# Kernel tuning notes

Hardware: AMD Instinct MI355X
Metric: run time of the kernel (lower is better)

## Reference

```python
import jax, jax.numpy as jnp
import numpy as np

DIM = 1024
INNER = int(DIM * 1.5)
EPS = 1e-6


def setup_inputs() -> dict:
    key = jax.random.key(0)
    ks = jax.random.split(key, 8)
    B, L, D = 4, 2048, DIM
    s1 = 1.0 / np.sqrt(D)
    s2 = 1.0 / np.sqrt(INNER)
    return {
        "x": jax.random.normal(ks[0], (B, L, D), jnp.float32),
        "W1": jax.random.normal(ks[1], (D, INNER), jnp.float32) * s1,
        "b1": jnp.zeros((INNER,), jnp.float32),
        "W2": jax.random.normal(ks[2], (INNER, 3 * D), jnp.float32) * s2,
        "b2": jnp.zeros((3 * D,), jnp.float32),
        "Wv": jax.random.normal(ks[3], (D, D), jnp.float32) * (0.5 * s1),
        "bv": jnp.zeros((D,), jnp.float32),
        "mix_weight": jnp.full((D,), 0.5, jnp.float32),
        "norm_weight": jnp.ones((D,), jnp.float32),
    }


def rmsnorm(x, w):
    norm = jnp.sqrt(jnp.mean(x * x, axis=-1, keepdims=True) + EPS)
    return x / norm * w


def reference(x, W1, b1, W2, b2, Wv, bv, mix_weight, norm_weight):
    B, L, D = x.shape
    h = jax.nn.silu(x @ W1 + b1)              # [B,L,inner]
    qkg = h @ W2 + b2                          # [B,L,3D]
    q, k, g = jnp.split(qkg, 3, axis=-1)
    scores = jnp.einsum('bld,bmd->blm', q, k) / jnp.sqrt(jnp.float32(D))
    attn = jax.nn.softmax(scores, axis=-1)
    v = (x @ Wv + bv) * jax.nn.sigmoid(g)      # gated values [B,L,D]
    global_info = jnp.einsum('blm,bmd->bld', attn, v)
    output = mix_weight * global_info + (1.0 - mix_weight) * x
    return rmsnorm(output, norm_weight)
```

## Files before the change

### kernel.cpp

```cpp
#include <hip/hip_runtime.h>
#include <hip/hip_bf16.h>
#include <stdint.h>


typedef __bf16 bf16x8 __attribute__((ext_vector_type(8)));
typedef float f32x4 __attribute__((ext_vector_type(4)));

__device__ __forceinline__ unsigned short f2bf(float f) {
    unsigned int u = __float_as_uint(f);
    u += 0x7fffu + ((u >> 16) & 1u);
    return (unsigned short)(u >> 16);
}
__device__ __forceinline__ float bf2f(unsigned short s) {
    return __uint_as_float(((unsigned int)s) << 16);
}
__device__ __forceinline__ void llds16(const void* g, void* l) {
    __builtin_amdgcn_global_load_lds(
        (const __attribute__((address_space(1))) void*)g,
        (__attribute__((address_space(3))) void*)l, 16, 0, 0);
}

__global__ __launch_bounds__(256) void cvt_f32_bf16(
    const float* __restrict__ in, unsigned short* __restrict__ out, long long n8) {
    long long i = (long long)blockIdx.x * 256 + threadIdx.x;
    if (i >= n8) return;
    float4 a = ((const float4*)in)[2 * i];
    float4 b = ((const float4*)in)[2 * i + 1];
    ushort4 p0, p1;
    p0.x = f2bf(a.x); p0.y = f2bf(a.y); p0.z = f2bf(a.z); p0.w = f2bf(a.w);
    p1.x = f2bf(b.x); p1.y = f2bf(b.y); p1.z = f2bf(b.z); p1.w = f2bf(b.w);
    ((ushort4*)out)[2 * i] = p0;
    ((ushort4*)out)[2 * i + 1] = p1;
}

__global__ __launch_bounds__(256) void transpose_cvt(
    const float* __restrict__ in, unsigned short* __restrict__ out, int R, int C) {
    __shared__ unsigned short tile[32][33];
    int c0 = blockIdx.x * 32, r0 = blockIdx.y * 32;
    int cc = threadIdx.x & 31, rr = threadIdx.x >> 5;
#pragma unroll
    for (int p = 0; p < 4; ++p) {
        int r = rr + p * 8;
        tile[r][cc] = f2bf(in[(size_t)(r0 + r) * C + c0 + cc]);
    }
    __syncthreads();
#pragma unroll
    for (int p = 0; p < 4; ++p) {
        int c = rr + p * 8;
        out[(size_t)(c0 + c) * R + r0 + cc] = tile[cc][c];
    }
}

template <int EPI>
__global__ __launch_bounds__(512, 1) void gemm3(
    const unsigned short* __restrict__ A, int lda, long long Abs,
    const unsigned short* __restrict__ B, int ldb, long long Bbs,
    int K,
    void* __restrict__ out, int ldo, long long Obs,
    const float* __restrict__ bias,
    const unsigned short* __restrict__ gate, int ldg,
    const float* __restrict__ xres, const float* __restrict__ mix,
    float scale) {
    extern __shared__ unsigned short lds[];
    constexpr int BUFU = 24576;
    const int tid = threadIdx.x;
    const int lane = tid & 63, wid = tid >> 6;
    const int wr = wid >> 1, wc = wid & 1;
    const int bm = blockIdx.y * 256, bn = blockIdx.x * 128;
    const int z = blockIdx.z;
    A += (long long)z * Abs;
    B += (long long)z * Bbs;
    const int NT = K >> 6;

    const int sr = tid >> 3, ss = tid & 7;
    size_t ag[4], bg[2];
#pragma unroll
    for (int j = 0; j < 4; ++j) {
        int r = j * 64 + sr;
        ag[j] = (size_t)(bm + r) * lda + (size_t)((ss ^ (r & 7)) * 8);
    }
#pragma unroll
    for (int j = 0; j < 2; ++j) {
        int r = j * 64 + sr;
        bg[j] = (size_t)(bn + r) * ldb + (size_t)((ss ^ (r & 7)) * 8);
    }
    const int aL = wid * 512;

    const int arow = wr * 64 + (lane & 15);
    const int brow = wc * 64 + (lane & 15);
    const int g4 = lane >> 4;
    const int sx0 = ((g4 ^ (lane & 7)) * 8);
    const int sx1 = (((4 + g4) ^ (lane & 7)) * 8);

    f32x4 acc[4][4] = {};

#pragma unroll
    for (int j = 0; j < 4; ++j) llds16(A + ag[j], &lds[j * 4096 + aL]);
#pragma unroll
    for (int j = 0; j < 2; ++j) llds16(B + bg[j], &lds[16384 + j * 4096 + aL]);
#pragma unroll
    for (int j = 0; j < 4; ++j) llds16(A + ag[j] + 64, &lds[BUFU + j * 4096 + aL]);
#pragma unroll
    for (int j = 0; j < 2; ++j)
        llds16(B + bg[j] + 64, &lds[BUFU + 16384 + j * 4096 + aL]);
    asm volatile("s_waitcnt vmcnt(6)" ::: "memory");
    __builtin_amdgcn_s_barrier();

    int bb = 0;
    for (int t = 0; t < NT; ++t) {
        const bool st = (t + 2 < NT);
        if (st) {
            const int tgt = (bb >= BUFU) ? bb - BUFU : bb + 2 * BUFU;
            const size_t k0 = (size_t)(t + 2) << 6;
#pragma unroll
            for (int j = 0; j < 4; ++j)
                llds16(A + ag[j] + k0, &lds[tgt + j * 4096 + aL]);
#pragma unroll
            for (int j = 0; j < 2; ++j)
                llds16(B + bg[j] + k0, &lds[tgt + 16384 + j * 4096 + aL]);
        }
        __builtin_amdgcn_sched_barrier(0);
        const unsigned short* Ab = &lds[bb];
        const unsigned short* Bb = &lds[bb + 16384];
        bf16x8 a0[4], a1[4], b0[4], b1[4];
#pragma unroll
        for (int i = 0; i < 4; ++i) {
            a0[i] = *(const bf16x8*)&Ab[(arow + i * 16) * 64 + sx0];
            a1[i] = *(const bf16x8*)&Ab[(arow + i * 16) * 64 + sx1];
            b0[i] = *(const bf16x8*)&Bb[(brow + i * 16) * 64 + sx0];
            b1[i] = *(const bf16x8*)&Bb[(brow + i * 16) * 64 + sx1];
        }
#pragma unroll
        for (int i = 0; i < 4; ++i)
#pragma unroll
            for (int j = 0; j < 4; ++j)
                acc[i][j] = __builtin_amdgcn_mfma_f32_16x16x32_bf16(
                    a0[i], b0[j], acc[i][j], 0, 0, 0);
#pragma unroll
        for (int i = 0; i < 4; ++i)
#pragma unroll
            for (int j = 0; j < 4; ++j)
                acc[i][j] = __builtin_amdgcn_mfma_f32_16x16x32_bf16(
                    a1[i], b1[j], acc[i][j], 0, 0, 0);
        asm volatile("s_waitcnt lgkmcnt(0)" ::: "memory");
        if (st) asm volatile("s_waitcnt vmcnt(6)" ::: "memory");
        else    asm volatile("s_waitcnt vmcnt(0)" ::: "memory");
        __builtin_amdgcn_s_barrier();
        bb = (bb == 2 * BUFU) ? 0 : bb + BUFU;
    }

    const int row0 = bm + wr * 64, col0 = bn + wc * 64;
#pragma unroll
    for (int i = 0; i < 4; ++i) {
#pragma unroll
        for (int j = 0; j < 4; ++j) {
            const int n = col0 + j * 16 + (lane & 15);
            const int mb = row0 + i * 16 + ((lane >> 4) << 2);
            f32x4 v = acc[i][j];
            if constexpr (EPI == 0 || EPI == 1) {
                float bs = bias[n];
                unsigned short* o = (unsigned short*)out;
#pragma unroll
                for (int q = 0; q < 4; ++q) {
                    float val = v[q] + bs;
                    if constexpr (EPI == 0) val = val / (1.f + __expf(-val));
                    o[(size_t)(mb + q) * ldo + n] = f2bf(val);
                }
            } else if constexpr (EPI == 2) {
                float bs = bias[n];
                ushort4 pk;
                unsigned short* pku = (unsigned short*)&pk;
#pragma unroll
                for (int q = 0; q < 4; ++q) {
                    int m = mb + q;
                    float g = bf2f(gate[(size_t)m * ldg + n]);
                    float val = (v[q] + bs) / (1.f + __expf(-g));
                    pku[q] = f2bf(val);
                }
                unsigned short* o = (unsigned short*)out;
                size_t oi = ((size_t)(mb >> 11) * 1024 + n) * 2048 + (mb & 2047);
                *(ushort4*)(o + oi) = pk;
            } else if constexpr (EPI == 3) {
                float* o = (float*)out + (size_t)z * Obs;
#pragma unroll
                for (int q = 0; q < 4; ++q)
                    o[(size_t)(mb + q) * ldo + n] = v[q] * scale;
            } else {
                float* o = (float*)out + (size_t)z * Obs;
                const float* xr = xres + (size_t)z * Obs;
                float mw = mix[n];
#pragma unroll
                for (int q = 0; q < 4; ++q)
                    o[(size_t)(mb + q) * ldo + n] =
                        mw * v[q] + (1.f - mw) * xr[(size_t)(mb + q) * ldo + n];
            }
        }
    }
}

__global__ __launch_bounds__(256) void softmax_inplace(float* __restrict__ scores) {
    const int L = 2048;
    float* sr = scores + (size_t)blockIdx.x * L;
    const int t = threadIdx.x, lane = t & 63, wid = t >> 6;
    float4 a = ((const float4*)sr)[2 * t];
    float4 b = ((const float4*)sr)[2 * t + 1];
    float vv[8] = {a.x, a.y, a.z, a.w, b.x, b.y, b.z, b.w};
    float mx = vv[0];
#pragma unroll
    for (int i = 1; i < 8; ++i) mx = fmaxf(mx, vv[i]);
#pragma unroll
    for (int off = 32; off; off >>= 1) mx = fmaxf(mx, __shfl_xor(mx, off));
    __shared__ float redm[4], reds[4];
    if (lane == 0) redm[wid] = mx;
    __syncthreads();
    mx = fmaxf(fmaxf(redm[0], redm[1]), fmaxf(redm[2], redm[3]));
    float s = 0.f;
#pragma unroll
    for (int i = 0; i < 8; ++i) {
        vv[i] = __expf(vv[i] - mx);
        s += vv[i];
    }
#pragma unroll
    for (int off = 32; off; off >>= 1) s += __shfl_xor(s, off);
    if (lane == 0) reds[wid] = s;
    __syncthreads();
    s = reds[0] + reds[1] + reds[2] + reds[3];
    float inv = 1.f / s;
    ushort4 p0, p1;
    unsigned short* pp0 = (unsigned short*)&p0;
    unsigned short* pp1 = (unsigned short*)&p1;
#pragma unroll
    for (int i = 0; i < 4; ++i) pp0[i] = f2bf(vv[i] * inv);
#pragma unroll
    for (int i = 0; i < 4; ++i) pp1[i] = f2bf(vv[4 + i] * inv);
    unsigned short* pr = (unsigned short*)sr;
    ((ushort4*)pr)[2 * t] = p0;
    ((ushort4*)pr)[2 * t + 1] = p1;
}

__global__ __launch_bounds__(256) void rmsnorm_inplace(
    float* __restrict__ io, const float* __restrict__ w) {
    const int D = 1024;
    float* r = io + (size_t)blockIdx.x * D;
    const int t = threadIdx.x, lane = t & 63, wid = t >> 6;
    float4 v = ((const float4*)r)[t];
    float ss = v.x * v.x + v.y * v.y + v.z * v.z + v.w * v.w;
#pragma unroll
    for (int off = 32; off; off >>= 1) ss += __shfl_xor(ss, off);
    __shared__ float red[4];
    if (lane == 0) red[wid] = ss;
    __syncthreads();
    ss = red[0] + red[1] + red[2] + red[3];
    float sc = rsqrtf(ss / (float)D + 1e-6f);
    float4 wv = ((const float4*)w)[t];
    v.x *= sc * wv.x; v.y *= sc * wv.y; v.z *= sc * wv.z; v.w *= sc * wv.w;
    ((float4*)r)[t] = v;
}

extern "C" void kernel_launch(void* const* d_in, const int* in_sizes, int n_in,
                              void* d_out, int out_size, void* d_ws, size_t ws_size,
                              hipStream_t stream) {
    const float* x = (const float*)d_in[0];
    const float* W1 = (const float*)d_in[1];
    const float* b1 = (const float*)d_in[2];
    const float* W2 = (const float*)d_in[3];
    const float* b2 = (const float*)d_in[4];
    const float* Wv = (const float*)d_in[5];
    const float* bv = (const float*)d_in[6];
    const float* mixw = (const float*)d_in[7];
    const float* normw = (const float*)d_in[8];
    float* out = (float*)d_out;

    const int L = 2048, D = 1024, INNER = 1536, BN4 = 4;
    const int M = BN4 * L;
    const int SMEM = 147456;

    (void)hipFuncSetAttribute(reinterpret_cast<const void*>(&gemm3<0>),
                              hipFuncAttributeMaxDynamicSharedMemorySize, SMEM);
    (void)hipFuncSetAttribute(reinterpret_cast<const void*>(&gemm3<1>),
                              hipFuncAttributeMaxDynamicSharedMemorySize, SMEM);
    (void)hipFuncSetAttribute(reinterpret_cast<const void*>(&gemm3<2>),
                              hipFuncAttributeMaxDynamicSharedMemorySize, SMEM);
    (void)hipFuncSetAttribute(reinterpret_cast<const void*>(&gemm3<3>),
                              hipFuncAttributeMaxDynamicSharedMemorySize, SMEM);
    (void)hipFuncSetAttribute(reinterpret_cast<const void*>(&gemm3<4>),
                              hipFuncAttributeMaxDynamicSharedMemorySize, SMEM);

    char* w = (char*)d_ws;
    auto carve = [&](size_t bytes) {
        void* p = (void*)w;
        w += (bytes + 255) & ~(size_t)255;
        return p;
    };
    unsigned short* xbf = (unsigned short*)carve((size_t)M * D * 2);
    unsigned short* w1t = (unsigned short*)carve((size_t)INNER * D * 2);
    unsigned short* w2t = (unsigned short*)carve((size_t)3 * D * INNER * 2);
    unsigned short* wvt = (unsigned short*)carve((size_t)D * D * 2);
    unsigned short* h = (unsigned short*)carve((size_t)M * INNER * 2);
    unsigned short* qkg = (unsigned short*)carve((size_t)M * 3 * D * 2);
    unsigned short* vt = (unsigned short*)carve((size_t)BN4 * D * L * 2);
    float* scores = (float*)carve((size_t)BN4 * L * L * 4);

    cvt_f32_bf16<<<(M * D) / 2048, 256, 0, stream>>>(x, xbf, (long long)M * D / 8);
    transpose_cvt<<<dim3(INNER / 32, D / 32), 256, 0, stream>>>(W1, w1t, D, INNER);
    transpose_cvt<<<dim3(3 * D / 32, INNER / 32), 256, 0, stream>>>(W2, w2t, INNER, 3 * D);
    transpose_cvt<<<dim3(D / 32, D / 32), 256, 0, stream>>>(Wv, wvt, D, D);
    gemm3<0><<<dim3(INNER / 128, M / 256, 1), 512, SMEM, stream>>>(
        xbf, D, 0, w1t, D, 0, D, h, INNER, 0, b1, nullptr, 0, nullptr, nullptr, 1.f);
    gemm3<1><<<dim3(3 * D / 128, M / 256, 1), 512, SMEM, stream>>>(
        h, INNER, 0, w2t, INNER, 0, INNER, qkg, 3 * D, 0, b2, nullptr, 0, nullptr,
        nullptr, 1.f);
    gemm3<2><<<dim3(D / 128, M / 256, 1), 512, SMEM, stream>>>(
        xbf, D, 0, wvt, D, 0, D, vt, L, 0, bv, qkg + 2 * D, 3 * D, nullptr, nullptr,
        1.f);
    gemm3<3><<<dim3(L / 128, L / 256, BN4), 512, SMEM, stream>>>(
        qkg, 3 * D, (long long)L * 3 * D, qkg + D, 3 * D, (long long)L * 3 * D, D,
        scores, L, (long long)L * L, nullptr, nullptr, 0, nullptr, nullptr, 0.03125f);
    softmax_inplace<<<BN4 * L, 256, 0, stream>>>(scores);
    gemm3<4><<<dim3(D / 128, L / 256, BN4), 512, SMEM, stream>>>(
        (const unsigned short*)scores, 2 * L, (long long)L * 2 * L, vt, L,
        (long long)D * L, L, out, D, (long long)L * D, nullptr, nullptr, 0, x, mixw,
        1.f);
    rmsnorm_inplace<<<M, 256, 0, stream>>>(out, normw);
}
```

Baseline: 311.0 us.

## Add 256x256-tile GEMM kernel with interleaved LDS prefetch for three GEMMs

Adds a new gemm8 kernel that uses 256x256 output tiles (8 waves, each 128x64) instead of 128x256. It double-buffers A and B in LDS and spreads the global-to-LDS loads across four sub-phases of each k-step, with setprio around the MFMA blocks. The W1, W2 and QK^T GEMMs now use this kernel, which raises arithmetic intensity per loaded byte and halves the grid size. The cost is more accumulator registers (128 floats per thread) and fewer blocks for the smaller GEMMs, which could hurt occupancy or tail behaviour.

```diff
diff --git a/kernel.cpp b/kernel.cpp
--- a/kernel.cpp
+++ b/kernel.cpp
@@ -48,6 +48,145 @@
     for (int p = 0; p < 4; ++p) {
         int c = rr + p * 8;
         out[(size_t)(c0 + c) * R + r0 + cc] = tile[cc][c];
+    }
+}
+
+template <int EPI>
+__global__ __launch_bounds__(512, 1) void gemm8(
+    const unsigned short* __restrict__ A, int lda, long long Abs,
+    const unsigned short* __restrict__ B, int ldb, long long Bbs,
+    int K,
+    void* __restrict__ out, int ldo, long long Obs,
+    const float* __restrict__ bias, float scale) {
+    extern __shared__ unsigned short lds[];
+    const int tid = threadIdx.x, lane = tid & 63, wid = tid >> 6;
+    const int wr = wid >> 2, wc = wid & 3;
+    const int bm = blockIdx.y * 256, bn = blockIdx.x * 256;
+    const int z = blockIdx.z;
+    A += (long long)z * Abs;
+    B += (long long)z * Bbs;
+    const int NT = K >> 6;
+
+    const int srow = tid >> 3;
+    const int swz = ((tid & 7) ^ (srow & 7)) * 8;
+    size_t ga[2][2], gb[2][2];
+#pragma unroll
+    for (int h = 0; h < 2; ++h)
+#pragma unroll
+        for (int c = 0; c < 2; ++c) {
+            ga[h][c] = (size_t)(bm + h * 128 + c * 64 + srow) * lda + swz;
+            gb[h][c] = (size_t)(bn + h * 128 + c * 64 + srow) * ldb + swz;
+        }
+    const int wl = wid * 512;
+
+    auto stA = [&](int k0, int h, int bb) {
+        llds16(A + ga[h][0] + k0, &lds[bb + h * 8192 + wl]);
+        llds16(A + ga[h][1] + k0, &lds[bb + h * 8192 + 4096 + wl]);
+    };
+    auto stB = [&](int k0, int h, int bb) {
+        llds16(B + gb[h][0] + k0, &lds[bb + 16384 + h * 8192 + wl]);
+        llds16(B + gb[h][1] + k0, &lds[bb + 16384 + h * 8192 + 4096 + wl]);
+    };
+
+    const int l15 = lane & 15, g4 = lane >> 4, l7 = lane & 7;
+    const int xs0 = (g4 ^ l7) * 8;
+    const int xs1 = ((4 + g4) ^ l7) * 8;
+    const int abase = wr * 8192 + l15 * 64;
+    const int bbase = 16384 + (wc >> 1) * 8192 + (wc & 1) * 4096 + l15 * 64;
+
+    f32x4 acc[8][4] = {};
+
+    stA(0, 0, 0); stA(0, 1, 0); stB(0, 0, 0); stB(0, 1, 0);
+    stB(64, 0, 32768); stB(64, 1, 32768);
+    asm volatile("s_waitcnt vmcnt(4)" ::: "memory");
+    __builtin_amdgcn_s_barrier();
+
+    for (int kt = 0; kt < NT; kt += 2) {
+        const bool st2 = (kt + 2) < NT;
+        const int kA1 = (kt + 1) << 6;
+        const int kN2 = (kt + 2) << 6;
+        const int kN3 = (kt + 3) << 6;
+#pragma unroll
+        for (int hb = 0; hb < 2; ++hb) {
+            const int bb = hb * 32768;
+            bf16x8 bfr[4][2];
+            bf16x8 afr[2][2];
+#pragma unroll
+            for (int q = 0; q < 4; ++q) {
+                if (q == 0) {
+#pragma unroll
+                    for (int n = 0; n < 4; ++n) {
+                        bfr[n][0] = *(const bf16x8*)&lds[bb + bbase + n * 1024 + xs0];
+                        bfr[n][1] = *(const bf16x8*)&lds[bb + bbase + n * 1024 + xs1];
+                    }
+                }
+#pragma unroll
+                for (int mq = 0; mq < 2; ++mq) {
+                    afr[mq][0] =
+                        *(const bf16x8*)&lds[bb + abase + (q * 2 + mq) * 1024 + xs0];
+                    afr[mq][1] =
+                        *(const bf16x8*)&lds[bb + abase + (q * 2 + mq) * 1024 + xs1];
+                }
+                if (hb == 0) {
+                    if (q == 0) stA(kA1, 0, 32768);
+                    else if (q == 1) stA(kA1, 1, 32768);
+                    else if (q == 2) { if (st2) stB(kN2, 0, 0); }
+                    else { if (st2) stB(kN2, 1, 0); }
+                } else {
+                    if (q == 0) { if (st2) stA(kN2, 0, 0); }
+                    else if (q == 1) { if (st2) stA(kN2, 1, 0); }
+                    else if (q == 2) { if (st2) stB(kN3, 0, 32768); }
+                    else { if (st2) stB(kN3, 1, 32768); }
+                }
+                __builtin_amdgcn_s_barrier();
+                asm volatile("s_waitcnt lgkmcnt(0)" ::: "memory");
+                __builtin_amdgcn_sched_barrier(0);
+                __builtin_amdgcn_s_setprio(1);
+#pragma unroll
+                for (int s = 0; s < 2; ++s)
+#pragma unroll
+                    for (int mq = 0; mq < 2; ++mq)
+#pragma unroll
+                        for (int n = 0; n < 4; ++n)
+                            acc[q * 2 + mq][n] =
+                                __builtin_amdgcn_mfma_f32_16x16x32_bf16(
+                                    afr[mq][s], bfr[n][s], acc[q * 2 + mq][n],
+                                    0, 0, 0);
+                __builtin_amdgcn_s_setprio(0);
+                __builtin_amdgcn_sched_barrier(0);
+                if (q == 3) {
+                    if (st2) asm volatile("s_waitcnt vmcnt(4)" ::: "memory");
+                    else     asm volatile("s_waitcnt vmcnt(0)" ::: "memory");
+                }
+                __builtin_amdgcn_s_barrier();
+            }
+        }
+    }
+
+    const int row0 = bm + wr * 128, col0 = bn + wc * 64;
+#pragma unroll
+    for (int m = 0; m < 8; ++m) {
+#pragma unroll
+        for (int n = 0; n < 4; ++n) {
+            const int nn = col0 + n * 16 + l15;
+            const int mb = row0 + m * 16 + g4 * 4;
+            f32x4 v = acc[m][n];
+            if constexpr (EPI == 0 || EPI == 1) {
+                float bs = bias[nn];
+                unsigned short* o = (unsigned short*)out;
+#pragma unroll
+                for (int qq = 0; qq < 4; ++qq) {
+                    float val = v[qq] + bs;
+                    if constexpr (EPI == 0) val = val / (1.f + __expf(-val));
+                    o[(size_t)(mb + qq) * ldo + nn] = f2bf(val);
+                }
+            } else {
+                float* o = (float*)out + (size_t)z * Obs;
+#pragma unroll
+                for (int qq = 0; qq < 4; ++qq)
+                    o[(size_t)(mb + qq) * ldo + nn] = v[qq] * scale;
+            }
+        }
     }
 }
 
@@ -157,16 +296,7 @@
             const int n = col0 + j * 16 + (lane & 15);
             const int mb = row0 + i * 16 + ((lane >> 4) << 2);
             f32x4 v = acc[i][j];
-            if constexpr (EPI == 0 || EPI == 1) {
-                float bs = bias[n];
-                unsigned short* o = (unsigned short*)out;
-#pragma unroll
-                for (int q = 0; q < 4; ++q) {
-                    float val = v[q] + bs;
-                    if constexpr (EPI == 0) val = val / (1.f + __expf(-val));
-                    o[(size_t)(mb + q) * ldo + n] = f2bf(val);
-                }
-            } else if constexpr (EPI == 2) {
+            if constexpr (EPI == 2) {
                 float bs = bias[n];
                 ushort4 pk;
                 unsigned short* pku = (unsigned short*)&pk;
@@ -180,11 +310,6 @@
                 unsigned short* o = (unsigned short*)out;
                 size_t oi = ((size_t)(mb >> 11) * 1024 + n) * 2048 + (mb & 2047);
                 *(ushort4*)(o + oi) = pk;
-            } else if constexpr (EPI == 3) {
-                float* o = (float*)out + (size_t)z * Obs;
-#pragma unroll
-                for (int q = 0; q < 4; ++q)
-                    o[(size_t)(mb + q) * ldo + n] = v[q] * scale;
             } else {
                 float* o = (float*)out + (size_t)z * Obs;
                 const float* xr = xres + (size_t)z * Obs;
@@ -273,18 +398,19 @@
 
     const int L = 2048, D = 1024, INNER = 1536, BN4 = 4;
     const int M = BN4 * L;
-    const int SMEM = 147456;
-
-    (void)hipFuncSetAttribute(reinterpret_cast<const void*>(&gemm3<0>),
-                              hipFuncAttributeMaxDynamicSharedMemorySize, SMEM);
-    (void)hipFuncSetAttribute(reinterpret_cast<const void*>(&gemm3<1>),
-                              hipFuncAttributeMaxDynamicSharedMemorySize, SMEM);
+    const int SMEM3 = 147456;
+    const int SMEM8 = 131072;
+
+    (void)hipFuncSetAttribute(reinterpret_cast<const void*>(&gemm8<0>),
+                              hipFuncAttributeMaxDynamicSharedMemorySize, SMEM8);
+    (void)hipFuncSetAttribute(reinterpret_cast<const void*>(&gemm8<1>),
+                              hipFuncAttributeMaxDynamicSharedMemorySize, SMEM8);
+    (void)hipFuncSetAttribute(reinterpret_cast<const void*>(&gemm8<3>),
+                              hipFuncAttributeMaxDynamicSharedMemorySize, SMEM8);
     (void)hipFuncSetAttribute(reinterpret_cast<const void*>(&gemm3<2>),
-                              hipFuncAttributeMaxDynamicSharedMemorySize, SMEM);
-    (void)hipFuncSetAttribute(reinterpret_cast<const void*>(&gemm3<3>),
-                              hipFuncAttributeMaxDynamicSharedMemorySize, SMEM);
+                              hipFuncAttributeMaxDynamicSharedMemorySize, SMEM3);
     (void)hipFuncSetAttribute(reinterpret_cast<const void*>(&gemm3<4>),
-                              hipFuncAttributeMaxDynamicSharedMemorySize, SMEM);
+                              hipFuncAttributeMaxDynamicSharedMemorySize, SMEM3);
 
     char* w = (char*)d_ws;
     auto carve = [&](size_t bytes) {
@@ -305,19 +431,18 @@
     transpose_cvt<<<dim3(INNER / 32, D / 32), 256, 0, stream>>>(W1, w1t, D, INNER);
     transpose_cvt<<<dim3(3 * D / 32, INNER / 32), 256, 0, stream>>>(W2, w2t, INNER, 3 * D);
     transpose_cvt<<<dim3(D / 32, D / 32), 256, 0, stream>>>(Wv, wvt, D, D);
-    gemm3<0><<<dim3(INNER / 128, M / 256, 1), 512, SMEM, stream>>>(
-        xbf, D, 0, w1t, D, 0, D, h, INNER, 0, b1, nullptr, 0, nullptr, nullptr, 1.f);
-    gemm3<1><<<dim3(3 * D / 128, M / 256, 1), 512, SMEM, stream>>>(
-        h, INNER, 0, w2t, INNER, 0, INNER, qkg, 3 * D, 0, b2, nullptr, 0, nullptr,
-        nullptr, 1.f);
-    gemm3<2><<<dim3(D / 128, M / 256, 1), 512, SMEM, stream>>>(
+    gemm8<0><<<dim3(INNER / 256, M / 256, 1), 512, SMEM8, stream>>>(
+        xbf, D, 0, w1t, D, 0, D, h, INNER, 0, b1, 1.f);
+    gemm8<1><<<dim3(3 * D / 256, M / 256, 1), 512, SMEM8, stream>>>(
+        h, INNER, 0, w2t, INNER, 0, INNER, qkg, 3 * D, 0, b2, 1.f);
+    gemm3<2><<<dim3(D / 128, M / 256, 1), 512, SMEM3, stream>>>(
         xbf, D, 0, wvt, D, 0, D, vt, L, 0, bv, qkg + 2 * D, 3 * D, nullptr, nullptr,
         1.f);
-    gemm3<3><<<dim3(L / 128, L / 256, BN4), 512, SMEM, stream>>>(
+    gemm8<3><<<dim3(L / 256, L / 256, BN4), 512, SMEM8, stream>>>(
         qkg, 3 * D, (long long)L * 3 * D, qkg + D, 3 * D, (long long)L * 3 * D, D,
-        scores, L, (long long)L * L, nullptr, nullptr, 0, nullptr, nullptr, 0.03125f);
+        scores, L, (long long)L * L, nullptr, 0.03125f);
     softmax_inplace<<<BN4 * L, 256, 0, stream>>>(scores);
-    gemm3<4><<<dim3(D / 128, L / 256, BN4), 512, SMEM, stream>>>(
+    gemm3<4><<<dim3(D / 128, L / 256, BN4), 512, SMEM3, stream>>>(
         (const unsigned short*)scores, 2 * L, (long long)L * 2 * L, vt, L,
         (long long)D * L, L, out, D, (long long)L * D, nullptr, nullptr, 0, x, mixw,
         1.f);
```

New measurement: 313.8 us. Within noise of the previous version (+0.9%).
